# Kernel tuning notes

Hardware: AMD Instinct MI355X
Metric: run time of the kernel (lower is better)

Reference implementation:

```python
import jax, jax.numpy as jnp
import numpy as np

NEG_SLOPE = 0.1
LN_EPS = 1e-5


def setup_inputs() -> dict:
    key = jax.random.key(0)
    ks = jax.random.split(key, 8)
    B, S, IN, OUT, H = 16, 1024, 512, 512, 8
    DH = OUT // H
    x = jax.random.normal(ks[0], (B, S, IN), dtype=jnp.float32)
    scale = 1.0 / np.sqrt(IN)
    # per-head projection weights, stored as [H, in, dh] so y = x @ W
    wq = jax.random.uniform(ks[1], (H, IN, DH), minval=-scale, maxval=scale, dtype=jnp.float32)
    wk = jax.random.uniform(ks[2], (H, IN, DH), minval=-scale, maxval=scale, dtype=jnp.float32)
    wv = jax.random.uniform(ks[3], (H, IN, DH), minval=-scale, maxval=scale, dtype=jnp.float32)
    scale_o = 1.0 / np.sqrt(OUT)
    w_out = jax.random.uniform(ks[4], (OUT, OUT), minval=-scale_o, maxval=scale_o, dtype=jnp.float32)
    b_out = jax.random.uniform(ks[5], (OUT,), minval=-scale_o, maxval=scale_o, dtype=jnp.float32)
    ln_gamma = jnp.ones((OUT,), dtype=jnp.float32)
    ln_beta = jnp.zeros((OUT,), dtype=jnp.float32)
    return {"x": x, "wq": wq, "wk": wk, "wv": wv, "w_out": w_out,
            "b_out": b_out, "ln_gamma": ln_gamma, "ln_beta": ln_beta}


def reference(x, wq, wk, wv, w_out, b_out, ln_gamma, ln_beta):
    B, S, _ = x.shape
    H, _, DH = wq.shape
    # per-head projections, vectorized over heads: [H, B, S, DH]
    q = jnp.einsum('bsf,hfd->hbsd', x, wq)
    k = jnp.einsum('bsf,hfd->hbsd', x, wk)
    v = jnp.einsum('bsf,hfd->hbsd', x, wv)
    # attention scores [H, B, S, S]
    att = jnp.einsum('hbsd,hbtd->hbst', q, k) / jnp.sqrt(jnp.float32(DH))
    # FAITHFUL to source: softmax over dim=0 of the per-head [B,S,S] tensor,
    # i.e. the BATCH axis (axis=1 in our [H,B,S,S] layout)
    att = jax.nn.softmax(att, axis=1)
    out = jnp.einsum('hbst,hbtd->hbsd', att, v)
    # concat heads -> [B, S, H*DH]
    heads_cat = jnp.transpose(out, (1, 2, 0, 3)).reshape(B, S, H * DH)
    y = heads_cat @ w_out + b_out
    # LayerNorm over last dim
    mu = jnp.mean(y, axis=-1, keepdims=True)
    var = jnp.var(y, axis=-1, keepdims=True)
    y = (y - mu) * jax.lax.rsqrt(var + LN_EPS) * ln_gamma + ln_beta
    # LeakyReLU(0.1)
    return jnp.where(y >= 0, y, NEG_SLOPE * y)
```

## Files before the change

### kernel.cpp

```cpp
#include <hip/hip_runtime.h>

typedef unsigned short u16;
typedef unsigned int uint;
typedef __attribute__((ext_vector_type(8))) short bf16x8;
typedef __attribute__((ext_vector_type(4))) float f32x4;

#define NBATCH 16
#define SDIM   1024
#define INDIM  512
#define OUTDIM 512
#define HEADS  8
#define DHEAD  64
#define MROWS  (NBATCH * SDIM)
#define KDIM   512
#define QSCALE (0.125f * 1.44269504088896340736f)

__device__ __forceinline__ u16 f2bf(float f) {
  union { float f; uint u; } v; v.f = f;
  uint u = v.u;
  return (u16)((u + 0x7FFFu + ((u >> 16) & 1u)) >> 16);
}

__device__ __forceinline__ uint pkbf(float a, float b) {
  return (uint)f2bf(a) | ((uint)f2bf(b) << 16);
}

__device__ __forceinline__ uint pkbf_fast(float a, float b) {
  union { float f; uint u; } ua, ub; ua.f = a; ub.f = b;
  return __builtin_amdgcn_perm(ub.u + 0x8000u, ua.u + 0x8000u, 0x07060302);
}

__device__ __forceinline__ float bf2f(u16 v) {
  union { uint u; float f; } c; c.u = (uint)v << 16;
  return c.f;
}

__device__ __forceinline__ void gload16(const void* g, void* l) {
  __builtin_amdgcn_global_load_lds(
      (const __attribute__((address_space(1))) uint*)g,
      (__attribute__((address_space(3))) uint*)l, 16, 0, 0);
}

__global__ __launch_bounds__(256) void prep_kernel(
    const float* __restrict__ x, const float* __restrict__ wq,
    const float* __restrict__ wk, const float* __restrict__ wv,
    const float* __restrict__ w_out,
    u16* __restrict__ xb, u16* __restrict__ W1T, u16* __restrict__ W2T) {
  int gid = blockIdx.x * blockDim.x + threadIdx.x;
  int stride = gridDim.x * blockDim.x;
  const int NX4 = MROWS * INDIM / 4;
  for (int i = gid; i < NX4; i += stride) {
    float4 v = ((const float4*)x)[i];
    ((ushort4*)xb)[i] = make_ushort4(f2bf(v.x), f2bf(v.y), f2bf(v.z), f2bf(v.w));
  }
  for (int i = gid; i < 3 * OUTDIM * INDIM; i += stride) {
    int n = i >> 9, f = i & 511;
    int proj = n >> 9, hd = n & 511, h = hd >> 6, d = hd & 63;
    const float* src = (proj == 0) ? wq : (proj == 1) ? wk : wv;
    float val = src[(h * INDIM + f) * DHEAD + d];
    if (proj == 0) val *= QSCALE;
    W1T[i] = f2bf(val);
  }
  for (int i = gid; i < OUTDIM * INDIM; i += stride) {
    int n = i >> 9, f = i & 511;
    W2T[i] = f2bf(w_out[f * OUTDIM + n]);
  }
}

template <int EPI>
__global__ __launch_bounds__(256) void gemm128(
    const u16* __restrict__ A, const u16* __restrict__ Bt,
    u16* __restrict__ Qb, u16* __restrict__ Kb, u16* __restrict__ VTb,
    float* __restrict__ Y) {
  __shared__ u16 As[128 * 32];
  __shared__ u16 Bs[128 * 32];
  const int tid = threadIdx.x;
  const int w = tid >> 6, lane = tid & 63;
  const int quad = lane >> 4, ln = lane & 15;
  const int wm = w >> 1, wn = w & 1;
  const int m0 = blockIdx.y * 128, n0 = blockIdx.x * 128;

  f32x4 zero4 = {0.f, 0.f, 0.f, 0.f};
  f32x4 acc[4][4];
  for (int i = 0; i < 4; i++)
    for (int j = 0; j < 4; j++) acc[i][j] = zero4;

  const char* Ag = (const char*)(A + (size_t)m0 * KDIM);
  const char* Bg = (const char*)(Bt + (size_t)n0 * KDIM);
  const int r0 = w * 16 + (lane >> 2);
  const int cb = (lane & 3) * 16;

  for (int kk = 0; kk < KDIM; kk += 32) {
    __syncthreads();
    gload16(Ag + (size_t)r0 * (KDIM * 2) + kk * 2 + cb, (char*)As + w * 1024);
    gload16(Ag + (size_t)(r0 + 64) * (KDIM * 2) + kk * 2 + cb, (char*)As + 4096 + w * 1024);
    gload16(Bg + (size_t)r0 * (KDIM * 2) + kk * 2 + cb, (char*)Bs + w * 1024);
    gload16(Bg + (size_t)(r0 + 64) * (KDIM * 2) + kk * 2 + cb, (char*)Bs + 4096 + w * 1024);
    __syncthreads();
    bf16x8 af[4], bfr[4];
    for (int mt = 0; mt < 4; mt++)
      af[mt] = *(const bf16x8*)&As[(wm * 64 + mt * 16 + ln) * 32 + quad * 8];
    for (int nt = 0; nt < 4; nt++)
      bfr[nt] = *(const bf16x8*)&Bs[(wn * 64 + nt * 16 + ln) * 32 + quad * 8];
    for (int mt = 0; mt < 4; mt++)
      for (int nt = 0; nt < 4; nt++)
        acc[mt][nt] = __builtin_amdgcn_mfma_f32_16x16x32_bf16(af[mt], bfr[nt], acc[mt][nt], 0, 0, 0);
  }

  for (int mt = 0; mt < 4; mt++) {
    int mbase = m0 + wm * 64 + mt * 16 + quad * 4;
    int b = mbase >> 10, sbase = mbase & 1023;
    for (int nt = 0; nt < 4; nt++) {
      f32x4 c = acc[mt][nt];
      int col = n0 + wn * 64 + nt * 16 + ln;
      if (EPI == 0) {
        int proj = n0 >> 9;
        int hd = col & 511, h = hd >> 6, d = hd & 63;
        if (proj == 2) {
          *(ushort4*)&VTb[((size_t)(h * 16 + b) * 64 + d) * 1024 + sbase] =
              make_ushort4(f2bf(c[0]), f2bf(c[1]), f2bf(c[2]), f2bf(c[3]));
        } else {
          u16* dst = (proj == 0) ? Qb : Kb;
          size_t base = ((size_t)(h * 16 + b) * 1024) * 64 + d;
          dst[base + (size_t)(sbase + 0) * 64] = f2bf(c[0]);
          dst[base + (size_t)(sbase + 1) * 64] = f2bf(c[1]);
          dst[base + (size_t)(sbase + 2) * 64] = f2bf(c[2]);
          dst[base + (size_t)(sbase + 3) * 64] = f2bf(c[3]);
        }
      } else {
        Y[(size_t)(mbase + 0) * OUTDIM + col] = c[0];
        Y[(size_t)(mbase + 1) * OUTDIM + col] = c[1];
        Y[(size_t)(mbase + 2) * OUTDIM + col] = c[2];
        Y[(size_t)(mbase + 3) * OUTDIM + col] = c[3];
      }
    }
  }
}

__global__ __launch_bounds__(512, 4) void attnA_kernel(
    const u16* __restrict__ Qb, const u16* __restrict__ Kb,
    u16* __restrict__ LinvX) {
  __shared__ u16 Qt[2 * 64 * 64];
  __shared__ u16 Kt[2 * 256 * 64];
  const int tid = threadIdx.x;
  const int w = tid >> 6, lane = tid & 63;
  const int quad = lane >> 4, ln = lane & 15;
  const int ws = w & 3, wt = w >> 2;
  const int h = blockIdx.x & 7;
  const int s0 = ((blockIdx.x >> 3) & 15) * 64;
  const int tq = blockIdx.x >> 7;
  const int t0 = tq * 256;
  const int srow = tid >> 3, sseg = tid & 7;

  const u16* Qh = Qb + (size_t)h * 16 * 65536;
  const u16* Kh = Kb + (size_t)h * 16 * 65536;

  f32x4 zero4 = {0.f, 0.f, 0.f, 0.f};
  f32x4 Lacc[8];
  for (int i = 0; i < 8; i++) Lacc[i] = zero4;

  {
    gload16(Qh + (size_t)(s0 + srow) * 64 + sseg * 8, (char*)Qt + w * 1024);
    const u16* Kg = Kh + (size_t)(t0 + srow) * 64 + sseg * 8;
    gload16(Kg,            (char*)Kt + w * 1024);
    gload16(Kg + 64 * 64,  (char*)Kt + 8192 + w * 1024);
    gload16(Kg + 128 * 64, (char*)Kt + 16384 + w * 1024);
    gload16(Kg + 192 * 64, (char*)Kt + 24576 + w * 1024);
  }

  for (int b = 0; b < 16; b++) {
    const int cur = b & 1;
    __syncthreads();
    if (b < 15) {
      const u16* Qg = Qh + (size_t)(b + 1) * 65536 + (size_t)(s0 + srow) * 64 + sseg * 8;
      const u16* Kg = Kh + (size_t)(b + 1) * 65536 + (size_t)(t0 + srow) * 64 + sseg * 8;
      char* Kd = (char*)Kt + (cur ^ 1) * 32768 + w * 1024;
      gload16(Qg, (char*)Qt + (cur ^ 1) * 8192 + w * 1024);
      gload16(Kg,            Kd);
      gload16(Kg + 64 * 64,  Kd + 8192);
      gload16(Kg + 128 * 64, Kd + 16384);
      gload16(Kg + 192 * 64, Kd + 24576);
    }
    const u16* Qr = &Qt[cur * 4096 + (ws * 16 + ln) * 64];
    bf16x8 q0 = *(const bf16x8*)&Qr[quad * 8];
    bf16x8 q1 = *(const bf16x8*)&Qr[32 + quad * 8];
    for (int tsub = 0; tsub < 8; tsub++) {
      const u16* Kr = &Kt[cur * 16384 + (wt * 128 + tsub * 16 + ln) * 64];
      f32x4 cc = zero4;
      cc = __builtin_amdgcn_mfma_f32_16x16x32_bf16(*(const bf16x8*)&Kr[quad * 8], q0, cc, 0, 0, 0);
      cc = __builtin_amdgcn_mfma_f32_16x16x32_bf16(*(const bf16x8*)&Kr[32 + quad * 8], q1, cc, 0, 0, 0);
      f32x4 L = Lacc[tsub];
      L[0] += __builtin_amdgcn_exp2f(cc[0]); L[1] += __builtin_amdgcn_exp2f(cc[1]);
      L[2] += __builtin_amdgcn_exp2f(cc[2]); L[3] += __builtin_amdgcn_exp2f(cc[3]);
      Lacc[tsub] = L;
    }
  }

  const int sg = s0 + ws * 16 + ln;
  for (int tsub = 0; tsub < 8; tsub++) {
    const int tc = tq * 16 + wt * 8 + tsub;
    f32x4 L = Lacc[tsub];
    uint2 pk = make_uint2(
        pkbf(__builtin_amdgcn_rcpf(L[0]), __builtin_amdgcn_rcpf(L[1])),
        pkbf(__builtin_amdgcn_rcpf(L[2]), __builtin_amdgcn_rcpf(L[3])));
    *(uint2*)&LinvX[(((size_t)(h * 64 + tc)) * 1024 + sg) * 16 + quad * 4] = pk;
  }
}

__global__ __launch_bounds__(256, 4) void attnB_kernel(
    const u16* __restrict__ Qb, const u16* __restrict__ Kb,
    const u16* __restrict__ VTb, const u16* __restrict__ LinvX,
    u16* __restrict__ hc) {
  __shared__ u16 Ks[2 * 32 * 64];
  __shared__ u16 Vs[2 * 64 * 32];
  __shared__ u16 Pp[4 * 2 * 16 * 40];
  const int tid = threadIdx.x;
  const int w = tid >> 6, lane = tid & 63;
  const int quad = lane >> 4, ln = lane & 15;
  const int h = blockIdx.x & 7, b = (blockIdx.x >> 3) & 15, sblk = blockIdx.x >> 7;
  const int ss0 = sblk * 128 + w * 32;
  const int krow = tid >> 3;
  const int ksw = ((tid & 7) ^ (krow & 7)) * 8;
  const int vrow = tid >> 2;
  const int vsw = ((tid & 3) ^ ((tid >> 3) & 3)) * 8;

  const u16* Kbase = Kb + (size_t)(h * 16 + b) * 65536;
  const u16* Vbase = VTb + (size_t)(h * 16 + b) * 65536;
  const u16* LinvH = LinvX + (size_t)h * 64 * 1024 * 16;

  f32x4 zero4 = {0.f, 0.f, 0.f, 0.f};
  bf16x8 qf[2][2];
  for (int a = 0; a < 2; a++) {
    const u16* Qp = Qb + ((size_t)(h * 16 + b) * 1024 + ss0 + a * 16 + ln) * 64;
    qf[a][0] = *(const bf16x8*)&Qp[quad * 8];
    qf[a][1] = *(const bf16x8*)&Qp[32 + quad * 8];
  }
  f32x4 o[2][4];
  for (int a = 0; a < 2; a++)
    for (int df = 0; df < 4; df++) o[a][df] = zero4;

  gload16(Kbase + (size_t)krow * 64 + ksw, (char*)Ks + w * 1024);
  gload16(Vbase + (size_t)vrow * 1024 + vsw, (char*)Vs + w * 1024);

  const int fsw = (quad ^ (ln & 7)) * 8;
  const int vfsw = (quad ^ ((ln >> 1) & 3)) * 8;

  for (int it = 0; it < 32; ++it) {
    const int cur = it & 1;
    const int t0 = it * 32;
    __syncthreads();
    if (it < 31) {
      gload16(Kbase + (size_t)(t0 + 32 + krow) * 64 + ksw,
              (char*)Ks + (cur ^ 1) * 4096 + w * 1024);
      gload16(Vbase + (size_t)vrow * 1024 + t0 + 32 + vsw,
              (char*)Vs + (cur ^ 1) * 4096 + w * 1024);
    }
    bf16x8 kf[2][2], vf[4];
    for (int tsub = 0; tsub < 2; tsub++) {
      const u16* Kr = &Ks[cur * 2048 + (tsub * 16 + ln) * 64];
      kf[tsub][0] = *(const bf16x8*)&Kr[fsw];
      kf[tsub][1] = *(const bf16x8*)&Kr[fsw ^ 32];
    }
    for (int df = 0; df < 4; df++)
      vf[df] = *(const bf16x8*)&Vs[cur * 2048 + (df * 16 + ln) * 32 + vfsw];

    for (int a = 0; a < 2; a++) {
      for (int tsub = 0; tsub < 2; tsub++) {
        const int tc = it * 2 + tsub;
        ushort4 lin = *(const ushort4*)&LinvH[
            (((size_t)tc) * 1024 + ss0 + a * 16 + ln) * 16 + quad * 4];
        f32x4 cc = zero4;
        cc = __builtin_amdgcn_mfma_f32_16x16x32_bf16(kf[tsub][0], qf[a][0], cc, 0, 0, 0);
        cc = __builtin_amdgcn_mfma_f32_16x16x32_bf16(kf[tsub][1], qf[a][1], cc, 0, 0, 0);
        float p0 = __builtin_amdgcn_exp2f(cc[0]) * bf2f(lin.x);
        float p1 = __builtin_amdgcn_exp2f(cc[1]) * bf2f(lin.y);
        float p2 = __builtin_amdgcn_exp2f(cc[2]) * bf2f(lin.z);
        float p3 = __builtin_amdgcn_exp2f(cc[3]) * bf2f(lin.w);
        uint2 pk = make_uint2(pkbf_fast(p0, p1), pkbf_fast(p2, p3));
        *(uint2*)&Pp[(w * 2 + a) * 640 + ln * 40 + tsub * 16 + quad * 4] = pk;
      }
      bf16x8 pa = *(const bf16x8*)&Pp[(w * 2 + a) * 640 + ln * 40 + quad * 8];
      for (int df = 0; df < 4; df++)
        o[a][df] = __builtin_amdgcn_mfma_f32_16x16x32_bf16(pa, vf[df], o[a][df], 0, 0, 0);
    }
  }

  for (int a = 0; a < 2; a++) {
    for (int df = 0; df < 4; df++) {
      f32x4 c = o[a][df];
      for (int r = 0; r < 4; r++) {
        int sg = ss0 + a * 16 + quad * 4 + r;
        hc[((size_t)(b * 1024 + sg)) * 512 + h * 64 + df * 16 + ln] = f2bf(c[r]);
      }
    }
  }
}

__global__ __launch_bounds__(256) void ln_kernel(
    const float* __restrict__ Y, const float* __restrict__ b_out,
    const float* __restrict__ gamma, const float* __restrict__ beta,
    float* __restrict__ out) {
  const int w = threadIdx.x >> 6, lane = threadIdx.x & 63;
  const int row = blockIdx.x * 4 + w;
  const float4* yr = (const float4*)(Y + (size_t)row * 512);
  float4 v0 = yr[lane], v1 = yr[64 + lane];
  float4 b0 = ((const float4*)b_out)[lane], b1 = ((const float4*)b_out)[64 + lane];
  v0.x += b0.x; v0.y += b0.y; v0.z += b0.z; v0.w += b0.w;
  v1.x += b1.x; v1.y += b1.y; v1.z += b1.z; v1.w += b1.w;
  float s  = v0.x + v0.y + v0.z + v0.w + v1.x + v1.y + v1.z + v1.w;
  float s2 = v0.x * v0.x + v0.y * v0.y + v0.z * v0.z + v0.w * v0.w +
             v1.x * v1.x + v1.y * v1.y + v1.z * v1.z + v1.w * v1.w;
  for (int off = 32; off; off >>= 1) {
    s += __shfl_xor(s, off);
    s2 += __shfl_xor(s2, off);
  }
  float mean = s * (1.0f / 512.0f);
  float var = s2 * (1.0f / 512.0f) - mean * mean;
  float rs = rsqrtf(var + 1e-5f);
  float4 g0 = ((const float4*)gamma)[lane], g1 = ((const float4*)gamma)[64 + lane];
  float4 e0 = ((const float4*)beta)[lane], e1 = ((const float4*)beta)[64 + lane];
  float4 o0, o1;
  o0.x = (v0.x - mean) * rs * g0.x + e0.x;  o0.y = (v0.y - mean) * rs * g0.y + e0.y;
  o0.z = (v0.z - mean) * rs * g0.z + e0.z;  o0.w = (v0.w - mean) * rs * g0.w + e0.w;
  o1.x = (v1.x - mean) * rs * g1.x + e1.x;  o1.y = (v1.y - mean) * rs * g1.y + e1.y;
  o1.z = (v1.z - mean) * rs * g1.z + e1.z;  o1.w = (v1.w - mean) * rs * g1.w + e1.w;
  o0.x = o0.x >= 0.f ? o0.x : 0.1f * o0.x;  o0.y = o0.y >= 0.f ? o0.y : 0.1f * o0.y;
  o0.z = o0.z >= 0.f ? o0.z : 0.1f * o0.z;  o0.w = o0.w >= 0.f ? o0.w : 0.1f * o0.w;
  o1.x = o1.x >= 0.f ? o1.x : 0.1f * o1.x;  o1.y = o1.y >= 0.f ? o1.y : 0.1f * o1.y;
  o1.z = o1.z >= 0.f ? o1.z : 0.1f * o1.z;  o1.w = o1.w >= 0.f ? o1.w : 0.1f * o1.w;
  ((float4*)out)[(size_t)row * 128 + lane] = o0;
  ((float4*)out)[(size_t)row * 128 + 64 + lane] = o1;
}

extern "C" void kernel_launch(void* const* d_in, const int* in_sizes, int n_in,
                              void* d_out, int out_size, void* d_ws, size_t ws_size,
                              hipStream_t stream) {
  const float* x      = (const float*)d_in[0];
  const float* wq     = (const float*)d_in[1];
  const float* wk     = (const float*)d_in[2];
  const float* wv     = (const float*)d_in[3];
  const float* w_out  = (const float*)d_in[4];
  const float* b_out  = (const float*)d_in[5];
  const float* gamma  = (const float*)d_in[6];
  const float* beta   = (const float*)d_in[7];
  float* out = (float*)d_out;

  char* ws = (char*)d_ws;
  size_t off = 0;
  u16* xb  = (u16*)(ws + off); off += (size_t)MROWS * INDIM * 2;
  u16* W1T = (u16*)(ws + off); off += (size_t)3 * OUTDIM * INDIM * 2;
  u16* W2T = (u16*)(ws + off); off += (size_t)OUTDIM * INDIM * 2;
  u16* Qb  = (u16*)(ws + off); off += (size_t)HEADS * NBATCH * SDIM * DHEAD * 2;
  u16* Kb  = (u16*)(ws + off); off += (size_t)HEADS * NBATCH * SDIM * DHEAD * 2;
  u16* VTb = (u16*)(ws + off); off += (size_t)HEADS * NBATCH * SDIM * DHEAD * 2;
  u16* hc  = (u16*)(ws + off); off += (size_t)MROWS * OUTDIM * 2;
  float* Yv = (float*)(ws + off);
  u16* LinvX = (u16*)Yv;

  prep_kernel<<<2048, 256, 0, stream>>>(x, wq, wk, wv, w_out, xb, W1T, W2T);
  gemm128<0><<<dim3(12, 128), 256, 0, stream>>>(xb, W1T, Qb, Kb, VTb, nullptr);
  attnA_kernel<<<512, 512, 0, stream>>>(Qb, Kb, LinvX);
  attnB_kernel<<<1024, 256, 0, stream>>>(Qb, Kb, VTb, LinvX, hc);
  gemm128<1><<<dim3(4, 128), 256, 0, stream>>>(hc, W2T, nullptr, nullptr, nullptr, Yv);
  ln_kernel<<<4096, 256, 0, stream>>>(Yv, b_out, gamma, beta, out);
}
```

Before: 258.6 us.

## Double attention key tile to 64 per iteration with new swizzled LDS layout

The batch-softmax attention kernel now processes 64 keys per loop iteration instead of 32, halving the number of iterations and barriers. K and V tiles are loaded as two half-tiles with a new XOR swizzle, and the P staging buffer gets a matching swizzled layout. Inverse-normalizer addresses are precomputed so only a per-iteration offset remains. LDS use per block grows, which may reduce occupancy, and V fragments are now re-read from LDS for each query sub-tile.

```diff
diff --git a/kernel.cpp b/kernel.cpp
--- a/kernel.cpp
+++ b/kernel.cpp
@@ -211,22 +211,29 @@
     const u16* __restrict__ Qb, const u16* __restrict__ Kb,
     const u16* __restrict__ VTb, const u16* __restrict__ LinvX,
     u16* __restrict__ hc) {
-  __shared__ u16 Ks[2 * 32 * 64];
-  __shared__ u16 Vs[2 * 64 * 32];
-  __shared__ u16 Pp[4 * 2 * 16 * 40];
+  __shared__ u16 Ks[2 * 4096];
+  __shared__ u16 Vs[2 * 4096];
+  __shared__ u16 Pp[4 * 1024];
   const int tid = threadIdx.x;
   const int w = tid >> 6, lane = tid & 63;
   const int quad = lane >> 4, ln = lane & 15;
   const int h = blockIdx.x & 7, b = (blockIdx.x >> 3) & 15, sblk = blockIdx.x >> 7;
   const int ss0 = sblk * 128 + w * 32;
-  const int krow = tid >> 3;
-  const int ksw = ((tid & 7) ^ (krow & 7)) * 8;
-  const int vrow = tid >> 2;
-  const int vsw = ((tid & 3) ^ ((tid >> 3) & 3)) * 8;
-
-  const u16* Kbase = Kb + (size_t)(h * 16 + b) * 65536;
-  const u16* Vbase = VTb + (size_t)(h * 16 + b) * 65536;
-  const u16* LinvH = LinvX + (size_t)h * 64 * 1024 * 16;
+
+  const int srow = tid >> 2;
+  const int sgA = (tid & 3) ^ (srow & 7);
+  const int sgB = (4 + (tid & 3)) ^ (srow & 7);
+  const char* Ksrc = (const char*)(Kb + (size_t)(h * 16 + b) * 65536) + srow * 128;
+  const char* Vsrc = (const char*)(VTb + (size_t)(h * 16 + b) * 65536) + srow * 2048;
+
+  const int e = ln & 7;
+  const int l0 = quad ^ e, l1 = (4 + quad) ^ e;
+  const int koff0 = (l0 >> 2) * 2048 + (l0 & 3) * 8;
+  const int koff1 = (l1 >> 2) * 2048 + (l1 & 3) * 8;
+  int pwo[4];
+  for (int tsub = 0; tsub < 4; tsub++)
+    pwo[tsub] = (((tsub * 2 + (quad >> 1)) ^ e) * 8) + (quad & 1) * 4;
+  u16* PwB = &Pp[w * 1024 + ln * 64];
 
   f32x4 zero4 = {0.f, 0.f, 0.f, 0.f};
   bf16x8 qf[2][2];
@@ -239,36 +246,40 @@
   for (int a = 0; a < 2; a++)
     for (int df = 0; df < 4; df++) o[a][df] = zero4;
 
-  gload16(Kbase + (size_t)krow * 64 + ksw, (char*)Ks + w * 1024);
-  gload16(Vbase + (size_t)vrow * 1024 + vsw, (char*)Vs + w * 1024);
-
-  const int fsw = (quad ^ (ln & 7)) * 8;
-  const int vfsw = (quad ^ ((ln >> 1) & 3)) * 8;
-
-  for (int it = 0; it < 32; ++it) {
+  const u16* LinvP = LinvX + ((size_t)h * 64 * 1024 + ss0 + ln) * 16 + quad * 4;
+
+  gload16(Ksrc + sgA * 16, (char*)Ks + w * 1024);
+  gload16(Ksrc + sgB * 16, (char*)Ks + 4096 + w * 1024);
+  gload16(Vsrc + sgA * 16, (char*)Vs + w * 1024);
+  gload16(Vsrc + sgB * 16, (char*)Vs + 4096 + w * 1024);
+
+  for (int it = 0; it < 16; ++it) {
     const int cur = it & 1;
-    const int t0 = it * 32;
     __syncthreads();
-    if (it < 31) {
-      gload16(Kbase + (size_t)(t0 + 32 + krow) * 64 + ksw,
-              (char*)Ks + (cur ^ 1) * 4096 + w * 1024);
-      gload16(Vbase + (size_t)vrow * 1024 + t0 + 32 + vsw,
-              (char*)Vs + (cur ^ 1) * 4096 + w * 1024);
-    }
-    bf16x8 kf[2][2], vf[4];
-    for (int tsub = 0; tsub < 2; tsub++) {
-      const u16* Kr = &Ks[cur * 2048 + (tsub * 16 + ln) * 64];
-      kf[tsub][0] = *(const bf16x8*)&Kr[fsw];
-      kf[tsub][1] = *(const bf16x8*)&Kr[fsw ^ 32];
-    }
-    for (int df = 0; df < 4; df++)
-      vf[df] = *(const bf16x8*)&Vs[cur * 2048 + (df * 16 + ln) * 32 + vfsw];
-
+    if (it < 15) {
+      const char* Kn = Ksrc + (size_t)(it + 1) * 8192;
+      const char* Vn = Vsrc + (size_t)(it + 1) * 128;
+      char* kd = (char*)Ks + (cur ^ 1) * 8192 + w * 1024;
+      char* vd = (char*)Vs + (cur ^ 1) * 8192 + w * 1024;
+      gload16(Kn + sgA * 16, kd);
+      gload16(Kn + sgB * 16, kd + 4096);
+      gload16(Vn + sgA * 16, vd);
+      gload16(Vn + sgB * 16, vd + 4096);
+    }
+    const u16* Kf = &Ks[cur * 4096 + ln * 32];
+    const u16* Vf = &Vs[cur * 4096 + ln * 32];
+    bf16x8 kf[4][2];
+#pragma unroll
+    for (int tsub = 0; tsub < 4; tsub++) {
+      kf[tsub][0] = *(const bf16x8*)&Kf[koff0 + tsub * 512];
+      kf[tsub][1] = *(const bf16x8*)&Kf[koff1 + tsub * 512];
+    }
+    const u16* Lit = LinvP + (size_t)it * 65536;
+#pragma unroll
     for (int a = 0; a < 2; a++) {
-      for (int tsub = 0; tsub < 2; tsub++) {
-        const int tc = it * 2 + tsub;
-        ushort4 lin = *(const ushort4*)&LinvH[
-            (((size_t)tc) * 1024 + ss0 + a * 16 + ln) * 16 + quad * 4];
+#pragma unroll
+      for (int tsub = 0; tsub < 4; tsub++) {
+        ushort4 lin = *(const ushort4*)&Lit[tsub * 16384 + a * 256];
         f32x4 cc = zero4;
         cc = __builtin_amdgcn_mfma_f32_16x16x32_bf16(kf[tsub][0], qf[a][0], cc, 0, 0, 0);
         cc = __builtin_amdgcn_mfma_f32_16x16x32_bf16(kf[tsub][1], qf[a][1], cc, 0, 0, 0);
@@ -276,12 +287,17 @@
         float p1 = __builtin_amdgcn_exp2f(cc[1]) * bf2f(lin.y);
         float p2 = __builtin_amdgcn_exp2f(cc[2]) * bf2f(lin.z);
         float p3 = __builtin_amdgcn_exp2f(cc[3]) * bf2f(lin.w);
-        uint2 pk = make_uint2(pkbf_fast(p0, p1), pkbf_fast(p2, p3));
-        *(uint2*)&Pp[(w * 2 + a) * 640 + ln * 40 + tsub * 16 + quad * 4] = pk;
+        *(uint2*)&PwB[pwo[tsub]] = make_uint2(pkbf_fast(p0, p1), pkbf_fast(p2, p3));
       }
-      bf16x8 pa = *(const bf16x8*)&Pp[(w * 2 + a) * 640 + ln * 40 + quad * 8];
-      for (int df = 0; df < 4; df++)
-        o[a][df] = __builtin_amdgcn_mfma_f32_16x16x32_bf16(pa, vf[df], o[a][df], 0, 0, 0);
+#pragma unroll
+      for (int c = 0; c < 2; c++) {
+        bf16x8 pa = *(const bf16x8*)&PwB[(c ? l1 : l0) * 8];
+#pragma unroll
+        for (int df = 0; df < 4; df++) {
+          bf16x8 vfr = *(const bf16x8*)&Vf[(c ? koff1 : koff0) + df * 512];
+          o[a][df] = __builtin_amdgcn_mfma_f32_16x16x32_bf16(pa, vfr, o[a][df], 0, 0, 0);
+        }
+      }
     }
   }
 
```

Result: slower. 271.8 us (+5.1%).

## Tile weight transposes through shared memory and store output projection as bf16

Applied to the files above, without the earlier changes.

The prep kernel now runs the weight transposes through a padded 64x64 shared-memory tile in dedicated blocks, instead of strided scalar gathers spread over every thread. The output-projection GEMM writes its intermediate Y in bf16 rather than fp32, and the LayerNorm kernel reads bf16 and converts back. This halves Y traffic and makes the weight loads and stores coalesced. The cost is rounding the pre-LayerNorm activations to bf16, which loses precision.

```diff
diff --git a/kernel.cpp b/kernel.cpp
--- a/kernel.cpp
+++ b/kernel.cpp
@@ -46,24 +46,45 @@
     const float* __restrict__ wk, const float* __restrict__ wv,
     const float* __restrict__ w_out,
     u16* __restrict__ xb, u16* __restrict__ W1T, u16* __restrict__ W2T) {
-  int gid = blockIdx.x * blockDim.x + threadIdx.x;
-  int stride = gridDim.x * blockDim.x;
-  const int NX4 = MROWS * INDIM / 4;
-  for (int i = gid; i < NX4; i += stride) {
-    float4 v = ((const float4*)x)[i];
-    ((ushort4*)xb)[i] = make_ushort4(f2bf(v.x), f2bf(v.y), f2bf(v.z), f2bf(v.w));
-  }
-  for (int i = gid; i < 3 * OUTDIM * INDIM; i += stride) {
-    int n = i >> 9, f = i & 511;
-    int proj = n >> 9, hd = n & 511, h = hd >> 6, d = hd & 63;
+  __shared__ float T[64 * 65];
+  const int tid = threadIdx.x;
+  if (blockIdx.x < 2048) {
+    const int NX4 = MROWS * INDIM / 4;
+    int stride = 2048 * 256;
+    for (int i = blockIdx.x * 256 + tid; i < NX4; i += stride) {
+      float4 v = ((const float4*)x)[i];
+      ((ushort4*)xb)[i] = make_ushort4(f2bf(v.x), f2bf(v.y), f2bf(v.z), f2bf(v.w));
+    }
+    return;
+  }
+  const int t = blockIdx.x - 2048;
+  const int rr = tid >> 6, cc = tid & 63;
+  if (t < 192) {
+    int proj = t >> 6, h = (t >> 3) & 7, f0 = (t & 7) * 64;
     const float* src = (proj == 0) ? wq : (proj == 1) ? wk : wv;
-    float val = src[(h * INDIM + f) * DHEAD + d];
-    if (proj == 0) val *= QSCALE;
-    W1T[i] = f2bf(val);
-  }
-  for (int i = gid; i < OUTDIM * INDIM; i += stride) {
-    int n = i >> 9, f = i & 511;
-    W2T[i] = f2bf(w_out[f * OUTDIM + n]);
+    float scale = (proj == 0) ? QSCALE : 1.0f;
+    for (int it = 0; it < 16; it++) {
+      int fi = it * 4 + rr;
+      T[fi * 65 + cc] = src[((size_t)h * 512 + f0 + fi) * 64 + cc] * scale;
+    }
+    __syncthreads();
+    u16* dst = W1T + ((size_t)(proj * 512 + h * 64)) * 512 + f0;
+    for (int it = 0; it < 16; it++) {
+      int d = it * 4 + rr;
+      dst[(size_t)d * 512 + cc] = f2bf(T[cc * 65 + d]);
+    }
+  } else {
+    int t2 = t - 192;
+    int n0 = (t2 >> 3) * 64, f0 = (t2 & 7) * 64;
+    for (int it = 0; it < 16; it++) {
+      int fi = it * 4 + rr;
+      T[fi * 65 + cc] = w_out[(size_t)(f0 + fi) * 512 + n0 + cc];
+    }
+    __syncthreads();
+    for (int it = 0; it < 16; it++) {
+      int ni = it * 4 + rr;
+      W2T[(size_t)(n0 + ni) * 512 + f0 + cc] = f2bf(T[cc * 65 + ni]);
+    }
   }
 }
 
@@ -71,7 +92,7 @@
 __global__ __launch_bounds__(256) void gemm128(
     const u16* __restrict__ A, const u16* __restrict__ Bt,
     u16* __restrict__ Qb, u16* __restrict__ Kb, u16* __restrict__ VTb,
-    float* __restrict__ Y) {
+    u16* __restrict__ Yb) {
   __shared__ u16 As[128 * 32];
   __shared__ u16 Bs[128 * 32];
   const int tid = threadIdx.x;
@@ -128,10 +149,10 @@
           dst[base + (size_t)(sbase + 3) * 64] = f2bf(c[3]);
         }
       } else {
-        Y[(size_t)(mbase + 0) * OUTDIM + col] = c[0];
-        Y[(size_t)(mbase + 1) * OUTDIM + col] = c[1];
-        Y[(size_t)(mbase + 2) * OUTDIM + col] = c[2];
-        Y[(size_t)(mbase + 3) * OUTDIM + col] = c[3];
+        Yb[(size_t)(mbase + 0) * OUTDIM + col] = f2bf(c[0]);
+        Yb[(size_t)(mbase + 1) * OUTDIM + col] = f2bf(c[1]);
+        Yb[(size_t)(mbase + 2) * OUTDIM + col] = f2bf(c[2]);
+        Yb[(size_t)(mbase + 3) * OUTDIM + col] = f2bf(c[3]);
       }
     }
   }
@@ -297,19 +318,21 @@
 }
 
 __global__ __launch_bounds__(256) void ln_kernel(
-    const float* __restrict__ Y, const float* __restrict__ b_out,
+    const u16* __restrict__ Yb, const float* __restrict__ b_out,
     const float* __restrict__ gamma, const float* __restrict__ beta,
     float* __restrict__ out) {
   const int w = threadIdx.x >> 6, lane = threadIdx.x & 63;
   const int row = blockIdx.x * 4 + w;
-  const float4* yr = (const float4*)(Y + (size_t)row * 512);
-  float4 v0 = yr[lane], v1 = yr[64 + lane];
-  float4 b0 = ((const float4*)b_out)[lane], b1 = ((const float4*)b_out)[64 + lane];
-  v0.x += b0.x; v0.y += b0.y; v0.z += b0.z; v0.w += b0.w;
-  v1.x += b1.x; v1.y += b1.y; v1.z += b1.z; v1.w += b1.w;
-  float s  = v0.x + v0.y + v0.z + v0.w + v1.x + v1.y + v1.z + v1.w;
-  float s2 = v0.x * v0.x + v0.y * v0.y + v0.z * v0.z + v0.w * v0.w +
-             v1.x * v1.x + v1.y * v1.y + v1.z * v1.z + v1.w * v1.w;
+  ushort4 ya = *(const ushort4*)&Yb[(size_t)row * 512 + lane * 8];
+  ushort4 yc = *(const ushort4*)&Yb[(size_t)row * 512 + lane * 8 + 4];
+  float4 b0 = ((const float4*)b_out)[lane * 2], b1 = ((const float4*)b_out)[lane * 2 + 1];
+  float v[8];
+  v[0] = bf2f(ya.x) + b0.x; v[1] = bf2f(ya.y) + b0.y;
+  v[2] = bf2f(ya.z) + b0.z; v[3] = bf2f(ya.w) + b0.w;
+  v[4] = bf2f(yc.x) + b1.x; v[5] = bf2f(yc.y) + b1.y;
+  v[6] = bf2f(yc.z) + b1.z; v[7] = bf2f(yc.w) + b1.w;
+  float s = 0.f, s2 = 0.f;
+  for (int j = 0; j < 8; j++) { s += v[j]; s2 += v[j] * v[j]; }
   for (int off = 32; off; off >>= 1) {
     s += __shfl_xor(s, off);
     s2 += __shfl_xor(s2, off);
@@ -317,19 +340,19 @@
   float mean = s * (1.0f / 512.0f);
   float var = s2 * (1.0f / 512.0f) - mean * mean;
   float rs = rsqrtf(var + 1e-5f);
-  float4 g0 = ((const float4*)gamma)[lane], g1 = ((const float4*)gamma)[64 + lane];
-  float4 e0 = ((const float4*)beta)[lane], e1 = ((const float4*)beta)[64 + lane];
-  float4 o0, o1;
-  o0.x = (v0.x - mean) * rs * g0.x + e0.x;  o0.y = (v0.y - mean) * rs * g0.y + e0.y;
-  o0.z = (v0.z - mean) * rs * g0.z + e0.z;  o0.w = (v0.w - mean) * rs * g0.w + e0.w;
-  o1.x = (v1.x - mean) * rs * g1.x + e1.x;  o1.y = (v1.y - mean) * rs * g1.y + e1.y;
-  o1.z = (v1.z - mean) * rs * g1.z + e1.z;  o1.w = (v1.w - mean) * rs * g1.w + e1.w;
-  o0.x = o0.x >= 0.f ? o0.x : 0.1f * o0.x;  o0.y = o0.y >= 0.f ? o0.y : 0.1f * o0.y;
-  o0.z = o0.z >= 0.f ? o0.z : 0.1f * o0.z;  o0.w = o0.w >= 0.f ? o0.w : 0.1f * o0.w;
-  o1.x = o1.x >= 0.f ? o1.x : 0.1f * o1.x;  o1.y = o1.y >= 0.f ? o1.y : 0.1f * o1.y;
-  o1.z = o1.z >= 0.f ? o1.z : 0.1f * o1.z;  o1.w = o1.w >= 0.f ? o1.w : 0.1f * o1.w;
-  ((float4*)out)[(size_t)row * 128 + lane] = o0;
-  ((float4*)out)[(size_t)row * 128 + 64 + lane] = o1;
+  float4 g0 = ((const float4*)gamma)[lane * 2], g1 = ((const float4*)gamma)[lane * 2 + 1];
+  float4 e0 = ((const float4*)beta)[lane * 2], e1 = ((const float4*)beta)[lane * 2 + 1];
+  float g[8] = {g0.x, g0.y, g0.z, g0.w, g1.x, g1.y, g1.z, g1.w};
+  float e[8] = {e0.x, e0.y, e0.z, e0.w, e1.x, e1.y, e1.z, e1.w};
+  float r[8];
+  for (int j = 0; j < 8; j++) {
+    float y = (v[j] - mean) * rs * g[j] + e[j];
+    r[j] = y >= 0.f ? y : 0.1f * y;
+  }
+  float4 o0 = make_float4(r[0], r[1], r[2], r[3]);
+  float4 o1 = make_float4(r[4], r[5], r[6], r[7]);
+  ((float4*)out)[(size_t)row * 128 + lane * 2] = o0;
+  ((float4*)out)[(size_t)row * 128 + lane * 2 + 1] = o1;
 }
 
 extern "C" void kernel_launch(void* const* d_in, const int* in_sizes, int n_in,
@@ -354,13 +377,13 @@
   u16* Kb  = (u16*)(ws + off); off += (size_t)HEADS * NBATCH * SDIM * DHEAD * 2;
   u16* VTb = (u16*)(ws + off); off += (size_t)HEADS * NBATCH * SDIM * DHEAD * 2;
   u16* hc  = (u16*)(ws + off); off += (size_t)MROWS * OUTDIM * 2;
-  float* Yv = (float*)(ws + off);
-  u16* LinvX = (u16*)Yv;
-
-  prep_kernel<<<2048, 256, 0, stream>>>(x, wq, wk, wv, w_out, xb, W1T, W2T);
+  u16* LinvX = (u16*)(ws + off);
+  u16* Yb = LinvX;
+
+  prep_kernel<<<2304, 256, 0, stream>>>(x, wq, wk, wv, w_out, xb, W1T, W2T);
   gemm128<0><<<dim3(12, 128), 256, 0, stream>>>(xb, W1T, Qb, Kb, VTb, nullptr);
   attnA_kernel<<<512, 512, 0, stream>>>(Qb, Kb, LinvX);
   attnB_kernel<<<1024, 256, 0, stream>>>(Qb, Kb, VTb, LinvX, hc);
-  gemm128<1><<<dim3(4, 128), 256, 0, stream>>>(hc, W2T, nullptr, nullptr, nullptr, Yv);
-  ln_kernel<<<4096, 256, 0, stream>>>(Yv, b_out, gamma, beta, out);
-}
+  gemm128<1><<<dim3(4, 128), 256, 0, stream>>>(hc, W2T, nullptr, nullptr, nullptr, Yb);
+  ln_kernel<<<4096, 256, 0, stream>>>(Yb, b_out, gamma, beta, out);
+}
```

Result: faster. 249.5 us (-3.5%).
